# Optimization experiments

Measured on AMD Instinct MI355X. Metric: run time of the kernel, lower is better.

The kernel has to match this reference:

```python
import jax, jax.numpy as jnp
import numpy as np

HEADS = 16
DIM_HEAD = 64
MAX_REL_POS = 1024   # temporal_length
TEXT_LEN = 77
IMG_SCALE = 1.0      # image_cross_attention_scale


def setup_inputs() -> dict:
    key = jax.random.key(0)
    ks = jax.random.split(key, 12)
    B, N, D = 32, 1024, 1024
    CTX = TEXT_LEN + 256
    s = 0.02
    return {
        "x": jax.random.normal(ks[0], (B, N, D), jnp.float32),
        "context": jax.random.normal(ks[1], (B, CTX, D), jnp.float32),
        "W_q": jax.random.normal(ks[2], (D, D), jnp.float32) * s,
        "W_k": jax.random.normal(ks[3], (D, D), jnp.float32) * s,
        "W_v": jax.random.normal(ks[4], (D, D), jnp.float32) * s,
        "W_k_ip": jax.random.normal(ks[5], (D, D), jnp.float32) * s,
        "W_v_ip": jax.random.normal(ks[6], (D, D), jnp.float32) * s,
        "rel_k": jax.random.normal(ks[7], (2 * MAX_REL_POS + 1, DIM_HEAD), jnp.float32) * s,
        "rel_v": jax.random.normal(ks[8], (2 * MAX_REL_POS + 1, DIM_HEAD), jnp.float32) * s,
        "W_out": jax.random.normal(ks[9], (D, D), jnp.float32) * s,
        "b_out": jnp.zeros((D,), jnp.float32),
        "alpha": jnp.zeros((1,), jnp.float32),
    }


def _split_heads(t):
    # [b, n, h*d] -> [b, h, n, d]
    b, n, _ = t.shape
    return t.reshape(b, n, HEADS, DIM_HEAD).transpose(0, 2, 1, 3)


def _merge_heads(t):
    # [b, h, n, d] -> [b, n, h*d]
    b, h, n, d = t.shape
    return t.transpose(0, 2, 1, 3).reshape(b, n, h * d)


def _rel_embeddings(table, len_q, len_k):
    # gather relative-position embeddings: [len_q, len_k, d]
    dist = jnp.arange(len_k)[None, :] - jnp.arange(len_q)[:, None]
    idx = jnp.clip(dist, -MAX_REL_POS, MAX_REL_POS) + MAX_REL_POS
    return table[idx]


def reference(x, context, W_q, W_k, W_v, W_k_ip, W_v_ip, rel_k, rel_v, W_out, b_out, alpha):
    scale = DIM_HEAD ** -0.5
    ctx_text = context[:, :TEXT_LEN, :]
    ctx_img = context[:, TEXT_LEN:, :]

    q = _split_heads(x @ W_q)          # [b,h,i,d]
    k = _split_heads(ctx_text @ W_k)   # [b,h,j,d]
    v = _split_heads(ctx_text @ W_v)

    sim = jnp.einsum('bhid,bhjd->bhij', q, k) * scale
    len_q, len_k = q.shape[2], k.shape[2]
    k2 = _rel_embeddings(rel_k, len_q, len_k)            # [i,j,d]
    sim = sim + jnp.einsum('bhid,ijd->bhij', q, k2) * scale
    attn = jax.nn.softmax(sim, axis=-1)

    out = jnp.einsum('bhij,bhjd->bhid', attn, v)
    v2 = _rel_embeddings(rel_v, len_q, len_k)            # [i,j,d]
    out = out + jnp.einsum('bhij,ijd->bhid', attn, v2)
    out = _merge_heads(out)                              # [b,i,h*d]

    # second image-context KV stream
    k_ip = _split_heads(ctx_img @ W_k_ip)
    v_ip = _split_heads(ctx_img @ W_v_ip)
    sim_ip = jnp.einsum('bhid,bhjd->bhij', q, k_ip) * scale
    attn_ip = jax.nn.softmax(sim_ip, axis=-1)
    out_ip = _merge_heads(jnp.einsum('bhij,bhjd->bhid', attn_ip, v_ip))

    # learnable-scale bypass: out + scale * out_ip * (tanh(alpha)+1)
    out = out + IMG_SCALE * out_ip * (jnp.tanh(alpha[0]) + 1.0)
    return out @ W_out + b_out
```

## Files before the change

### kernel.cpp

```cpp
#include <hip/hip_runtime.h>
#include <math.h>

typedef __bf16 bf16_t;
typedef __bf16 bf16x2 __attribute__((ext_vector_type(2)));
typedef __bf16 bf16x8 __attribute__((ext_vector_type(8)));
typedef float f32x4 __attribute__((ext_vector_type(4)));

#define BATCH   32
#define SEQ     1024
#define DMODEL  1024
#define NHEADS  16
#define DIMH    64
#define TEXTLEN 77
#define IMGLEN  256
#define CTXLEN  333
#define MAXREL  1024

#define MFMA16(a,b,c) __builtin_amdgcn_mfma_f32_16x16x32_bf16(a, b, c, 0, 0, 0)
#define SCALE_LOG2E 0.1803368809f

__device__ __forceinline__ unsigned pk2(float a, float b) {
  union { bf16x2 v; unsigned u; } t;
  t.v[0] = (bf16_t)a; t.v[1] = (bf16_t)b;
  return t.u;
}

__global__ __launch_bounds__(128) void k_cvt_ctx(const float* __restrict__ ctx,
                                                 bf16_t* __restrict__ ctxT,
                                                 bf16_t* __restrict__ ctxI) {
  int row = blockIdx.x;
  int b = row / CTXLEN, t = row - b * CTXLEN;
  const float* src = ctx + (size_t)row * DMODEL + threadIdx.x * 8;
  bf16_t* dst = (t < TEXTLEN)
      ? ctxT + ((size_t)(b * 80 + t)) * DMODEL + threadIdx.x * 8
      : ctxI + ((size_t)(b * IMGLEN + (t - TEXTLEN))) * DMODEL + threadIdx.x * 8;
  float4 a = *(const float4*)(src);
  float4 c = *(const float4*)(src + 4);
  bf16x8 o;
  o[0] = (bf16_t)a.x; o[1] = (bf16_t)a.y; o[2] = (bf16_t)a.z; o[3] = (bf16_t)a.w;
  o[4] = (bf16_t)c.x; o[5] = (bf16_t)c.y; o[6] = (bf16_t)c.z; o[7] = (bf16_t)c.w;
  *(bf16x8*)dst = o;
  if (t == 0) {
    bf16x8 z = {};
    #pragma unroll
    for (int rr = 77; rr < 80; ++rr)
      *(bf16x8*)(ctxT + ((size_t)(b * 80 + rr)) * DMODEL + threadIdx.x * 8) = z;
  }
}

__global__ void k_transpose_w(const float* __restrict__ W, bf16_t* __restrict__ WT) {
  __shared__ float tile[32][33];
  int x = threadIdx.x, y = threadIdx.y;
  int n0 = blockIdx.x * 32, k0 = blockIdx.y * 32;
  #pragma unroll
  for (int r = 0; r < 32; r += 8)
    tile[y + r][x] = W[(size_t)(k0 + y + r) * DMODEL + n0 + x];
  __syncthreads();
  #pragma unroll
  for (int r = 0; r < 32; r += 8)
    WT[(size_t)(n0 + y + r) * DMODEL + k0 + x] = (bf16_t)tile[x][y + r];
}

__global__ __launch_bounds__(256) void k_cvt_relk(const float* __restrict__ relk,
                                                  bf16_t* __restrict__ Rkb) {
  int idx = blockIdx.x * 256 + threadIdx.x;
  int u = idx >> 3, d0 = (idx & 7) * 8;
  const float* s = relk + (size_t)(u + 1) * DIMH + d0;
  float4 a = *(const float4*)s;
  float4 b = *(const float4*)(s + 4);
  bf16x8 o;
  o[0] = (bf16_t)a.x; o[1] = (bf16_t)a.y; o[2] = (bf16_t)a.z; o[3] = (bf16_t)a.w;
  o[4] = (bf16_t)b.x; o[5] = (bf16_t)b.y; o[6] = (bf16_t)b.z; o[7] = (bf16_t)b.w;
  *(bf16x8*)(Rkb + (size_t)u * DIMH + d0) = o;
}

__global__ __launch_bounds__(256) void k_cvt_relvT(const float* __restrict__ relv,
                                                   bf16_t* __restrict__ RvT) {
  int idx = blockIdx.x * 256 + threadIdx.x;
  int d = idx >> 8, u0 = (idx & 255) * 8;
  bf16x8 o;
  #pragma unroll
  for (int e = 0; e < 8; ++e)
    o[e] = (bf16_t)relv[(size_t)(u0 + e + 1) * DIMH + d];
  *(bf16x8*)(RvT + (size_t)d * 2048 + u0) = o;
}

typedef __attribute__((address_space(1))) void gvoid;
typedef __attribute__((address_space(3))) void svoid;

__device__ __forceinline__ void async_ld16(const void* g, void* l) {
  __builtin_amdgcn_global_load_lds((gvoid*)g, (svoid*)l, 16, 0, 0);
}

template<int STORE, bool AF32, bool AHM>
__global__ __launch_bounds__(256) void k_gemm(
    const void* __restrict__ Ain, const bf16_t* __restrict__ BT,
    void* __restrict__ Cout, void* __restrict__ Cout2,
    const float* __restrict__ bias, int M, int N, int K)
{
  constexpr int ABYTES = AF32 ? 16384 : 8192;
  __shared__ __align__(16) char lds_a[ABYTES];
  __shared__ __align__(16) bf16_t lds_b[128 * 32];
  const int tid = threadIdx.x;
  const int wid = tid >> 6, lane = tid & 63;
  const int nx = gridDim.x, ny = gridDim.y;
  const int lin = blockIdx.y * nx + blockIdx.x;
  const int nwg = nx * ny;
  const int swz = (lin & 7) * (nwg >> 3) + (lin >> 3);
  const int bcol = (swz % ny) * 128;
  const int brow = (swz / ny) * 128;
  const int wr = (wid >> 1) * 64, wc = (wid & 1) * 64;
  const int lhi = lane >> 4, llo = lane & 15;

  f32x4 acc[4][4];
  #pragma unroll
  for (int m = 0; m < 4; ++m)
    #pragma unroll
    for (int n = 0; n < 4; ++n)
      acc[m][n] = (f32x4){0.f, 0.f, 0.f, 0.f};

  for (int kk = 0; kk < K; kk += 32) {
    if constexpr (AF32) {
      const float* A32 = (const float*)Ain;
      #pragma unroll
      for (int q = 0; q < 4; ++q) {
        int base = q * 4096 + wid * 1024;
        int L = base + lane * 16;
        int row = L >> 7, col16 = (L >> 4) & 7;
        async_ld16(A32 + (size_t)(brow + row) * K + kk + ((col16 ^ (row & 7)) << 2),
                   lds_a + base);
      }
    } else if constexpr (AHM) {
      const bf16_t* A16 = (const bf16_t*)Ain;
      const int hh = kk >> 6;
      #pragma unroll
      for (int ch = 0; ch < 2; ++ch) {
        int e = wid * 512 + ch * 2048 + lane * 8;
        int row = e >> 5, col = e & 31;
        int grow = brow + row;
        const bf16_t* src = A16
            + (((size_t)((grow >> 10) * 16 + hh) * 1024 + (grow & 1023)) << 6)
            + (kk & 32) + col;
        async_ld16(src, lds_a + (size_t)(wid * 512 + ch * 2048) * 2);
      }
    } else {
      const bf16_t* A16 = (const bf16_t*)Ain;
      #pragma unroll
      for (int ch = 0; ch < 2; ++ch) {
        int e = wid * 512 + ch * 2048 + lane * 8;
        int row = e >> 5, col = e & 31;
        async_ld16(A16 + (size_t)(brow + row) * K + kk + col,
                   lds_a + (size_t)(wid * 512 + ch * 2048) * 2);
      }
    }
    #pragma unroll
    for (int ch = 0; ch < 2; ++ch) {
      int e = wid * 512 + ch * 2048 + lane * 8;
      int row = e >> 5, col = e & 31;
      async_ld16(BT + (size_t)(bcol + row) * K + kk + col, &lds_b[wid * 512 + ch * 2048]);
    }
    __syncthreads();
    bf16x8 af[4], bfv[4];
    if constexpr (AF32) {
      #pragma unroll
      for (int m = 0; m < 4; ++m) {
        int row = wr + m * 16 + llo;
        int sw = (llo & 7) << 4;
        const char* rp = lds_a + row * 128;
        f32x4 a0 = *(const f32x4*)(rp + (((lhi * 2) << 4) ^ sw));
        f32x4 a1 = *(const f32x4*)(rp + (((lhi * 2 + 1) << 4) ^ sw));
        bf16x8 v;
        v[0] = (bf16_t)a0[0]; v[1] = (bf16_t)a0[1]; v[2] = (bf16_t)a0[2]; v[3] = (bf16_t)a0[3];
        v[4] = (bf16_t)a1[0]; v[5] = (bf16_t)a1[1]; v[6] = (bf16_t)a1[2]; v[7] = (bf16_t)a1[3];
        af[m] = v;
      }
    } else {
      #pragma unroll
      for (int m = 0; m < 4; ++m)
        af[m] = *(const bf16x8*)(lds_a + (size_t)((wr + m * 16 + llo) * 32 + lhi * 8) * 2);
    }
    #pragma unroll
    for (int n = 0; n < 4; ++n)
      bfv[n] = *(const bf16x8*)&lds_b[(wc + n * 16 + llo) * 32 + lhi * 8];
    #pragma unroll
    for (int m = 0; m < 4; ++m)
      #pragma unroll
      for (int n = 0; n < 4; ++n)
        acc[m][n] = MFMA16(af[m], bfv[n], acc[m][n]);
    __syncthreads();
  }

  #pragma unroll
  for (int m = 0; m < 4; ++m)
    #pragma unroll
    for (int n = 0; n < 4; ++n) {
      const int gc = bcol + wc + n * 16 + llo;
      #pragma unroll
      for (int r = 0; r < 4; ++r) {
        const int gr = brow + wr + m * 16 + lhi * 4 + r;
        float v = acc[m][n][r];
        if constexpr (STORE == 2) {
          ((float*)Cout)[(size_t)gr * N + gc] = v + bias[gc];
        } else if constexpr (STORE == 4) {
          int hh2 = gc >> 6;
          ((bf16_t*)Cout)[((((size_t)((gr >> 10) * 16 + hh2)) << 10) + (gr & 1023)) * 64
                          + (gc & 63)] = (bf16_t)v;
        } else if constexpr (STORE == 5) {
          int bb = (gr * 6554) >> 19;
          int jj = gr - bb * 80;
          int hh2 = (gc & 1023) >> 6;
          bf16_t* dst = (gc < 1024) ? (bf16_t*)Cout : (bf16_t*)Cout2;
          dst[(((size_t)(bb * 16 + hh2) * 80 + jj) << 6) + (gc & 63)] = (bf16_t)v;
        } else {
          int bb = gr >> 8, uu = gr & 255;
          int hh2 = (gc & 1023) >> 6;
          bf16_t* dst = (gc < 1024) ? (bf16_t*)Cout : (bf16_t*)Cout2;
          dst[((((size_t)(bb * 16 + hh2)) << 8) + uu) * 64 + (gc & 63)] = (bf16_t)v;
        }
      }
    }
}

template<int RPB, int OUTC>
__global__ __launch_bounds__(256) void k_vtrans(const bf16_t* __restrict__ V,
                                                bf16_t* __restrict__ Vt) {
  __shared__ bf16_t tile[64][72];
  const int nt = (OUTC + 63) / 64;
  const int u0 = (blockIdx.x % nt) * 64;
  const int bh = blockIdx.x / nt;
  const int tid = threadIdx.x;
  const int ur = tid >> 2, cg = (tid & 3) * 16;
  {
    const bf16_t* src = V + (((size_t)bh * RPB + u0 + ur) << 6) + cg;
    *(bf16x8*)&tile[ur][cg] = *(const bf16x8*)src;
    *(bf16x8*)&tile[ur][cg + 8] = *(const bf16x8*)(src + 8);
  }
  __syncthreads();
  bf16x8 o0, o1;
  #pragma unroll
  for (int e = 0; e < 8; ++e) { o0[e] = tile[cg + e][ur]; o1[e] = tile[cg + 8 + e][ur]; }
  bf16_t* dst = Vt + (size_t)bh * 64 * OUTC + (size_t)ur * OUTC + u0 + cg;
  if (u0 + cg + 8 <= OUTC)  *(bf16x8*)dst = o0;
  if (u0 + cg + 16 <= OUTC) *(bf16x8*)(dst + 8) = o1;
}

__global__ __launch_bounds__(256, 2) void k_txt(
    const bf16_t* __restrict__ Qh,
    const bf16_t* __restrict__ Kth,
    const bf16_t* __restrict__ Vtt,
    const bf16_t* __restrict__ Rkb,
    const bf16_t* __restrict__ RvT,
    bf16_t* __restrict__ Oh)
{
  __shared__ __align__(16) bf16_t kt_l[80 * 64];
  __shared__ __align__(16) bf16_t vt_l[64 * 80];
  __shared__ __align__(16) char p_l[4][6400];
  __shared__ __align__(16) char qlds[4][2048];
  __shared__ __align__(16) char olds[4][2048];
  const int tid = threadIdx.x;
  const int w = tid >> 6, lane = tid & 63;
  const int c = lane & 15, g = lane >> 4;
  const int bh = blockIdx.x;

  #pragma unroll
  for (int q = 0; q < 3; ++q) {
    int cid0 = q * 256 + w * 64;
    if (cid0 < 640) {
      int cid = cid0 + lane;
      int row = cid >> 3, cc = cid & 7;
      const bf16_t* src = Kth + (((size_t)bh * 80 + row) << 6) + ((cc ^ (row & 7)) << 3);
      async_ld16(src, (char*)kt_l + cid0 * 16);
    }
  }
  #pragma unroll
  for (int q = 0; q < 3; ++q) {
    int cid0 = q * 256 + w * 64;
    if (cid0 < 640) {
      int cid = cid0 + lane;
      int row = cid / 10;
      int col = cid - row * 10;
      int colp = col - (row & 7); if (colp < 0) colp += 10;
      const bf16_t* src = Vtt + (size_t)bh * 5120 + row * 80 + colp * 8;
      async_ld16(src, (char*)vt_l + cid0 * 16);
    }
  }
  {
    int iq = w * 256;
    #pragma unroll
    for (int k2 = 0; k2 < 2; ++k2) {
      int k = k2 * 64 + lane, rr = k >> 3, cc = k & 7;
      async_ld16(Qh + (((size_t)bh * 1024 + iq + rr) << 6) + ((cc ^ (rr & 7)) << 3),
                 qlds[w] + k2 * 1024);
    }
  }
  __syncthreads();

  bf16_t* p = (bf16_t*)p_l[w];

  for (int st = 0; st < 16; ++st) {
    const int iq = w * 256 + st * 16;
    const int ub = 1008 - iq;
    asm volatile("s_waitcnt vmcnt(0)" ::: "memory");
    bf16x8 qa0 = *(const bf16x8*)(qlds[w] + c * 128 + ((g ^ (c & 7)) << 4));
    bf16x8 qa1 = *(const bf16x8*)(qlds[w] + c * 128 + (((g + 4) ^ (c & 7)) << 4));
    asm volatile("s_waitcnt lgkmcnt(0)" ::: "memory");
    if (st < 15) {
      int iqn = iq + 16;
      #pragma unroll
      for (int k2 = 0; k2 < 2; ++k2) {
        int k = k2 * 64 + lane, rr = k >> 3, cc = k & 7;
        async_ld16(Qh + (((size_t)bh * 1024 + iqn + rr) << 6) + ((cc ^ (rr & 7)) << 3),
                   qlds[w] + k2 * 1024);
      }
    }
    f32x4 ta[6];
    #pragma unroll
    for (int n = 0; n < 6; ++n) ta[n] = (f32x4){0.f, 0.f, 0.f, 0.f};
    {
      const bf16_t* rp = Rkb + (size_t)(ub + c) * DIMH + g * 8;
      #pragma unroll
      for (int n = 0; n < 6; ++n) {
        bf16x8 b0 = *(const bf16x8*)(rp + n * 16 * DIMH);
        bf16x8 b1 = *(const bf16x8*)(rp + n * 16 * DIMH + 32);
        ta[n] = MFMA16(qa0, b0, ta[n]);
        ta[n] = MFMA16(qa1, b1, ta[n]);
      }
    }
    f32x4 s[5];
    #pragma unroll
    for (int n = 0; n < 5; ++n) s[n] = (f32x4){0.f, 0.f, 0.f, 0.f};
    {
      const int sw = (c & 7) << 4;
      #pragma unroll
      for (int n = 0; n < 5; ++n) {
        int rb = (n * 16 + c) * 128;
        bf16x8 k0 = *(const bf16x8*)((const char*)kt_l + rb + ((g << 4) ^ sw));
        bf16x8 k1 = *(const bf16x8*)((const char*)kt_l + rb + (((4 + g) << 4) ^ sw));
        s[n] = MFMA16(qa0, k0, s[n]);
        s[n] = MFMA16(qa1, k1, s[n]);
      }
    }
    float st4[5][4];
    #pragma unroll
    for (int r = 0; r < 4; ++r) {
      int il = 4 * g + r;
      int cz = c + 15 - il;
      int srcl = (lane & 48) | (cz & 15);
      bool lo_pick = (cz >> 4) == 0;
      #pragma unroll
      for (int n = 0; n < 5; ++n) {
        float tlo = __shfl(ta[n][r], srcl);
        float thi = __shfl(ta[n + 1][r], srcl);
        float tv = lo_pick ? tlo : thi;
        int j = 16 * n + c;
        st4[n][r] = (j < TEXTLEN) ? (s[n][r] + tv) : -1e30f;
      }
    }
    float rsum[4];
    #pragma unroll
    for (int r = 0; r < 4; ++r) {
      float m = st4[0][r];
      #pragma unroll
      for (int n = 1; n < 5; ++n) m = fmaxf(m, st4[n][r]);
      m = fmaxf(m, __shfl_xor(m, 1));
      m = fmaxf(m, __shfl_xor(m, 2));
      m = fmaxf(m, __shfl_xor(m, 4));
      m = fmaxf(m, __shfl_xor(m, 8));
      float ssum = 0.f;
      #pragma unroll
      for (int n = 0; n < 5; ++n) {
        float pv = exp2f((st4[n][r] - m) * SCALE_LOG2E);
        st4[n][r] = pv;
        ssum += pv;
      }
      ssum += __shfl_xor(ssum, 1);
      ssum += __shfl_xor(ssum, 2);
      ssum += __shfl_xor(ssum, 4);
      ssum += __shfl_xor(ssum, 8);
      rsum[r] = ssum;
    }
    {
      bf16x8 z8 = {};
      #pragma unroll
      for (int z = 0; z < 7; ++z) {
        int off = z * 1024 + lane * 16;
        if (off < 6400)
          *(bf16x8*)((char*)p + off) = z8;
      }
      #pragma unroll
      for (int n = 0; n < 5; ++n)
        #pragma unroll
        for (int r = 0; r < 4; ++r) {
          int j = 16 * n + c;
          if (j < TEXTLEN) {
            int il = 4 * g + r;
            bf16_t pb = (bf16_t)st4[n][r];
            p[il * 200 + (j + 15 - il)] = pb;
            p[il * 200 + 96 + j] = pb;
          }
        }
    }
    f32x4 ot[4];
    #pragma unroll
    for (int dt = 0; dt < 4; ++dt) ot[dt] = (f32x4){0.f, 0.f, 0.f, 0.f};
    #pragma unroll
    for (int kt = 0; kt < 6; ++kt) {
      bf16x8 pf = *(const bf16x8*)(p + c * 200 + kt * 32 + g * 8);
      int klo = kt * 32 + g * 8;
      #pragma unroll
      for (int dt = 0; dt < 4; ++dt) {
        int d = dt * 16 + c;
        bf16x8 af;
        if (klo < 96) {
          af = *(const bf16x8*)(RvT + (size_t)d * 2048 + ub + klo);
        } else {
          int uv = klo - 96;
          int chunk = (uv >> 3) + (c & 7); if (chunk >= 10) chunk -= 10;
          af = *(const bf16x8*)((const char*)vt_l + d * 160 + chunk * 16);
        }
        ot[dt] = MFMA16(af, pf, ot[dt]);
      }
    }
    int srcq = ((c >> 2) << 4) | c;
    float t0 = __shfl(rsum[0], srcq);
    float t1 = __shfl(rsum[1], srcq);
    float t2 = __shfl(rsum[2], srcq);
    float t3 = __shfl(rsum[3], srcq);
    float rs = (c & 2) ? ((c & 1) ? t3 : t2) : ((c & 1) ? t1 : t0);
    float inv = 1.f / rs;
    #pragma unroll
    for (int dt = 0; dt < 4; ++dt) {
      int chunk = dt * 2 + (g >> 1);
      char* pa = olds[w] + c * 128 + ((chunk ^ (c & 7)) << 4) + (g & 1) * 8;
      uint2 nv;
      nv.x = pk2(ot[dt][0] * inv, ot[dt][1] * inv);
      nv.y = pk2(ot[dt][2] * inv, ot[dt][3] * inv);
      *(uint2*)pa = nv;
    }
    char* ob = (char*)(Oh + (((size_t)bh * 1024 + iq) << 6));
    #pragma unroll
    for (int k2 = 0; k2 < 2; ++k2) {
      int k = k2 * 64 + lane, rr = k >> 3, cc = k & 7;
      uint4 v = *(uint4*)(olds[w] + rr * 128 + ((cc ^ (rr & 7)) << 4));
      *(uint4*)(ob + rr * 128 + cc * 16) = v;
    }
  }
}

__global__ __launch_bounds__(256, 2) void k_img(
    const bf16_t* __restrict__ Qh,
    const bf16_t* __restrict__ Khi,
    const bf16_t* __restrict__ Vipt,
    const float* __restrict__ alpha,
    bf16_t* __restrict__ Oh)
{
  __shared__ __align__(16) bf16_t kst[256 * 64];
  __shared__ __align__(16) bf16_t vst[64 * 256];
  __shared__ __align__(16) char qlds[4][2048];
  __shared__ __align__(16) char olds[4][2048];
  const int tid = threadIdx.x;
  const int w = tid >> 6, lane = tid & 63;
  const int c = lane & 15, g = lane >> 4;
  const int i0 = blockIdx.x * 512;
  const int bh = blockIdx.y;

  #pragma unroll
  for (int q = 0; q < 8; ++q) {
    int cid = q * 256 + tid;
    int row = cid >> 3, cc = cid & 7;
    const bf16_t* src = Khi + (((size_t)bh * 256 + row) << 6) + ((cc ^ (row & 7)) << 3);
    async_ld16(src, (char*)kst + q * 4096 + w * 1024);
  }
  const char* vsrc0 = (const char*)(Vipt + (size_t)bh * 16384);
  #pragma unroll
  for (int q = 0; q < 8; ++q) {
    int L = (q * 256 + tid) * 16;
    int row = L >> 9;
    async_ld16(vsrc0 + (L ^ ((row & 7) << 4)), (char*)vst + q * 4096 + w * 1024);
  }
  {
    int iq = i0 + w * 128;
    #pragma unroll
    for (int k2 = 0; k2 < 2; ++k2) {
      int k = k2 * 64 + lane, rr = k >> 3, cc = k & 7;
      size_t off = (((size_t)bh * 1024 + iq + rr) << 6) + ((cc ^ (rr & 7)) << 3);
      async_ld16(Qh + off, qlds[w] + k2 * 1024);
      async_ld16(Oh + off, olds[w] + k2 * 1024);
    }
  }
  __syncthreads();

  const float coef = tanhf(alpha[0]) + 1.0f;

  for (int st = 0; st < 8; ++st) {
    const int iq = i0 + w * 128 + st * 16;
    asm volatile("s_waitcnt vmcnt(0)" ::: "memory");
    bf16x8 qa0 = *(const bf16x8*)(qlds[w] + c * 128 + ((g ^ (c & 7)) << 4));
    bf16x8 qa1 = *(const bf16x8*)(qlds[w] + c * 128 + (((g + 4) ^ (c & 7)) << 4));
    asm volatile("s_waitcnt lgkmcnt(0)" ::: "memory");
    if (st < 7) {
      int iqn = iq + 16;
      #pragma unroll
      for (int k2 = 0; k2 < 2; ++k2) {
        int k = k2 * 64 + lane, rr = k >> 3, cc = k & 7;
        async_ld16(Qh + (((size_t)bh * 1024 + iqn + rr) << 6) + ((cc ^ (rr & 7)) << 3),
                   qlds[w] + k2 * 1024);
      }
    }
    f32x4 acc[4];
    #pragma unroll
    for (int dt = 0; dt < 4; ++dt) acc[dt] = (f32x4){0.f, 0.f, 0.f, 0.f};
    float m_run = -1e30f, l_run = 0.f;

    #pragma unroll
    for (int jt = 0; jt < 2; ++jt) {
      f32x4 s2[8];
      #pragma unroll
      for (int n = 0; n < 8; ++n) s2[n] = (f32x4){0.f, 0.f, 0.f, 0.f};
      const int sw = (c & 7) << 4;
      #pragma unroll
      for (int n = 0; n < 8; ++n) {
        int rb = (jt * 128 + n * 16 + c) * 128;
        bf16x8 k0 = *(const bf16x8*)((const char*)kst + rb + ((g << 4) ^ sw));
        bf16x8 k1 = *(const bf16x8*)((const char*)kst + rb + (((4 + g) << 4) ^ sw));
        s2[n] = MFMA16(k0, qa0, s2[n]);
        s2[n] = MFMA16(k1, qa1, s2[n]);
      }
      float mx = -1e30f;
      #pragma unroll
      for (int n = 0; n < 8; ++n)
        #pragma unroll
        for (int r = 0; r < 4; ++r) mx = fmaxf(mx, s2[n][r]);
      mx = fmaxf(mx, __shfl_xor(mx, 16));
      mx = fmaxf(mx, __shfl_xor(mx, 32));
      float m_new = fmaxf(m_run, mx);
      float fscale = exp2f((m_run - m_new) * SCALE_LOG2E);
      float tsum = 0.f;
      #pragma unroll
      for (int n = 0; n < 8; ++n)
        #pragma unroll
        for (int r = 0; r < 4; ++r) {
          float pv = exp2f((s2[n][r] - m_new) * SCALE_LOG2E);
          s2[n][r] = pv; tsum += pv;
        }
      tsum += __shfl_xor(tsum, 16);
      tsum += __shfl_xor(tsum, 32);
      l_run = l_run * fscale + tsum;
      m_run = m_new;
      #pragma unroll
      for (int dt = 0; dt < 4; ++dt) acc[dt] *= fscale;
      const int srcA = c | ((g & 1) << 5);
      const int srcB = srcA + 16;
      const bool hi_n = ((g >> 1) & 1) != 0;
      #pragma unroll
      for (int kt = 0; kt < 4; ++kt) {
        unsigned lo0 = pk2(s2[2 * kt][0], s2[2 * kt][1]);
        unsigned hi0 = pk2(s2[2 * kt][2], s2[2 * kt][3]);
        unsigned lo1 = pk2(s2[2 * kt + 1][0], s2[2 * kt + 1][1]);
        unsigned hi1 = pk2(s2[2 * kt + 1][2], s2[2 * kt + 1][3]);
        unsigned a0 = __shfl(lo0, srcA), a1 = __shfl(lo1, srcA);
        unsigned b0 = __shfl(hi0, srcA), b1 = __shfl(hi1, srcA);
        unsigned c0 = __shfl(lo0, srcB), c1 = __shfl(lo1, srcB);
        unsigned d0 = __shfl(hi0, srcB), d1 = __shfl(hi1, srcB);
        union { unsigned u[4]; bf16x8 v; } pf;
        pf.u[0] = hi_n ? a1 : a0;
        pf.u[1] = hi_n ? b1 : b0;
        pf.u[2] = hi_n ? c1 : c0;
        pf.u[3] = hi_n ? d1 : d0;
        #pragma unroll
        for (int dt = 0; dt < 4; ++dt) {
          int d = dt * 16 + c;
          int a = (d * 512 + jt * 256 + kt * 64 + g * 16) ^ ((c & 7) << 4);
          bf16x8 vf = *(const bf16x8*)((const char*)vst + a);
          acc[dt] = MFMA16(vf, pf.v, acc[dt]);
        }
      }
    }
    float inv = coef / l_run;
    asm volatile("s_waitcnt vmcnt(0)" ::: "memory");
    #pragma unroll
    for (int dt = 0; dt < 4; ++dt) {
      int chunk = dt * 2 + (g >> 1);
      char* pa = olds[w] + c * 128 + ((chunk ^ (c & 7)) << 4) + (g & 1) * 8;
      union { uint2 u2; bf16_t e[4]; } ov; ov.u2 = *(uint2*)pa;
      uint2 nv;
      nv.x = pk2((float)ov.e[0] + acc[dt][0] * inv, (float)ov.e[1] + acc[dt][1] * inv);
      nv.y = pk2((float)ov.e[2] + acc[dt][2] * inv, (float)ov.e[3] + acc[dt][3] * inv);
      *(uint2*)pa = nv;
    }
    char* ob = (char*)(Oh + (((size_t)bh * 1024 + iq) << 6));
    #pragma unroll
    for (int k2 = 0; k2 < 2; ++k2) {
      int k = k2 * 64 + lane, rr = k >> 3, cc = k & 7;
      uint4 v = *(uint4*)(olds[w] + rr * 128 + ((cc ^ (rr & 7)) << 4));
      *(uint4*)(ob + rr * 128 + cc * 16) = v;
    }
    asm volatile("s_waitcnt lgkmcnt(0)" ::: "memory");
    if (st < 7) {
      int iqn = iq + 16;
      #pragma unroll
      for (int k2 = 0; k2 < 2; ++k2) {
        int k = k2 * 64 + lane, rr = k >> 3, cc = k & 7;
        async_ld16(Oh + (((size_t)bh * 1024 + iqn + rr) << 6) + ((cc ^ (rr & 7)) << 3),
                   olds[w] + k2 * 1024);
      }
    }
  }
}

extern "C" void kernel_launch(void* const* d_in, const int* in_sizes, int n_in,
                              void* d_out, int out_size, void* d_ws, size_t ws_size,
                              hipStream_t stream)
{
  const float* x     = (const float*)d_in[0];
  const float* ctx   = (const float*)d_in[1];
  const float* W_q   = (const float*)d_in[2];
  const float* W_k   = (const float*)d_in[3];
  const float* W_v   = (const float*)d_in[4];
  const float* W_kip = (const float*)d_in[5];
  const float* W_vip = (const float*)d_in[6];
  const float* rel_k = (const float*)d_in[7];
  const float* rel_v = (const float*)d_in[8];
  const float* W_out = (const float*)d_in[9];
  const float* b_out = (const float*)d_in[10];
  const float* alpha = (const float*)d_in[11];

  char* ws = (char*)d_ws;
  bf16_t* Oh   = (bf16_t*)(ws + 0);
  bf16_t* Qh   = (bf16_t*)(ws + 67108864);
  bf16_t* CtxT = (bf16_t*)(ws + 134217728);
  bf16_t* CtxI = (bf16_t*)(ws + 139460608);
  bf16_t* WTs  = (bf16_t*)(ws + 156237824);
  bf16_t* WqT   = WTs + 0 * 1048576;
  bf16_t* WkT   = WTs + 1 * 1048576;
  bf16_t* WvT   = WTs + 2 * 1048576;
  bf16_t* WkipT = WTs + 3 * 1048576;
  bf16_t* WvipT = WTs + 4 * 1048576;
  bf16_t* WoutT = WTs + 5 * 1048576;

  char* dob = (char*)d_out;
  bf16_t* Khi   = (bf16_t*)(dob + 0);
  bf16_t* Vhi   = (bf16_t*)(dob + 16777216);
  bf16_t* Vipt  = (bf16_t*)(dob + 33554432);
  bf16_t* Kth   = (bf16_t*)(dob + 50331648);
  bf16_t* Vth   = (bf16_t*)(dob + 55574528);
  bf16_t* Vtt   = (bf16_t*)(dob + 60817408);
  bf16_t* Rkb   = (bf16_t*)(dob + 66060288);
  bf16_t* RvT   = (bf16_t*)(dob + 66322432);

  k_cvt_ctx<<<BATCH * CTXLEN, 128, 0, stream>>>(ctx, CtxT, CtxI);
  dim3 tb(32, 8), tg(32, 32);
  k_transpose_w<<<tg, tb, 0, stream>>>(W_q,   WqT);
  k_transpose_w<<<tg, tb, 0, stream>>>(W_k,   WkT);
  k_transpose_w<<<tg, tb, 0, stream>>>(W_v,   WvT);
  k_transpose_w<<<tg, tb, 0, stream>>>(W_kip, WkipT);
  k_transpose_w<<<tg, tb, 0, stream>>>(W_vip, WvipT);
  k_transpose_w<<<tg, tb, 0, stream>>>(W_out, WoutT);
  k_cvt_relk<<<64, 256, 0, stream>>>(rel_k, Rkb);
  k_cvt_relvT<<<64, 256, 0, stream>>>(rel_v, RvT);

  k_gemm<4, true,  false><<<dim3(256, 8), 256, 0, stream>>>(x, WqT, (void*)Qh, nullptr, nullptr, 32768, 1024, 1024);
  k_gemm<5, false, false><<<dim3(20, 16), 256, 0, stream>>>(CtxT, WkT,   (void*)Kth, (void*)Vth, nullptr, 2560, 2048, 1024);
  k_gemm<6, false, false><<<dim3(64, 16), 256, 0, stream>>>(CtxI, WkipT, (void*)Khi, (void*)Vhi, nullptr, 8192, 2048, 1024);

  k_vtrans<80,  80 ><<<2 * 512, 256, 0, stream>>>(Vth, Vtt);
  k_vtrans<256, 256><<<4 * 512, 256, 0, stream>>>(Vhi, Vipt);

  k_txt<<<512, 256, 0, stream>>>(Qh, Kth, Vtt, Rkb, RvT, Oh);
  k_img<<<dim3(2, 512), 256, 0, stream>>>(Qh, Khi, Vipt, alpha, Oh);

  k_gemm<2, false, true><<<dim3(256, 8), 256, 0, stream>>>(Oh, WoutT, d_out, nullptr, b_out, 32768, 1024, 1024);
}
```

Measured before the change: 583.1 us.

## Double-buffer LDS tiles in GEMM to overlap global loads with MFMA

The GEMM kernel now keeps two LDS buffers for the A and B tiles and issues the async global-to-LDS loads for the next K step before computing on the current one. Explicit vmcnt waits, matched to the number of outstanding loads per stage, replace the full syncthreads, so memory latency can overlap MFMA work. This doubles LDS use per block, which may lower occupancy, and it relies on hand-counted waitcnt values being correct.

```diff
diff --git a/kernel.cpp b/kernel.cpp
--- a/kernel.cpp
+++ b/kernel.cpp
@@ -99,8 +99,8 @@
     const float* __restrict__ bias, int M, int N, int K)
 {
   constexpr int ABYTES = AF32 ? 16384 : 8192;
-  __shared__ __align__(16) char lds_a[ABYTES];
-  __shared__ __align__(16) bf16_t lds_b[128 * 32];
+  __shared__ __align__(16) char lds_a[2][ABYTES];
+  __shared__ __align__(16) bf16_t lds_b[2][128 * 32];
   const int tid = threadIdx.x;
   const int wid = tid >> 6, lane = tid & 63;
   const int nx = gridDim.x, ny = gridDim.y;
@@ -112,14 +112,8 @@
   const int wr = (wid >> 1) * 64, wc = (wid & 1) * 64;
   const int lhi = lane >> 4, llo = lane & 15;
 
-  f32x4 acc[4][4];
-  #pragma unroll
-  for (int m = 0; m < 4; ++m)
-    #pragma unroll
-    for (int n = 0; n < 4; ++n)
-      acc[m][n] = (f32x4){0.f, 0.f, 0.f, 0.f};
-
-  for (int kk = 0; kk < K; kk += 32) {
+  auto stage = [&](int kk, int buf) __attribute__((always_inline)) {
+    char* la = lds_a[buf];
     if constexpr (AF32) {
       const float* A32 = (const float*)Ain;
       #pragma unroll
@@ -128,7 +122,7 @@
         int L = base + lane * 16;
         int row = L >> 7, col16 = (L >> 4) & 7;
         async_ld16(A32 + (size_t)(brow + row) * K + kk + ((col16 ^ (row & 7)) << 2),
-                   lds_a + base);
+                   la + base);
       }
     } else if constexpr (AHM) {
       const bf16_t* A16 = (const bf16_t*)Ain;
@@ -141,7 +135,7 @@
         const bf16_t* src = A16
             + (((size_t)((grow >> 10) * 16 + hh) * 1024 + (grow & 1023)) << 6)
             + (kk & 32) + col;
-        async_ld16(src, lds_a + (size_t)(wid * 512 + ch * 2048) * 2);
+        async_ld16(src, la + (size_t)(wid * 512 + ch * 2048) * 2);
       }
     } else {
       const bf16_t* A16 = (const bf16_t*)Ain;
@@ -150,23 +144,48 @@
         int e = wid * 512 + ch * 2048 + lane * 8;
         int row = e >> 5, col = e & 31;
         async_ld16(A16 + (size_t)(brow + row) * K + kk + col,
-                   lds_a + (size_t)(wid * 512 + ch * 2048) * 2);
-      }
-    }
+                   la + (size_t)(wid * 512 + ch * 2048) * 2);
+      }
+    }
+    bf16_t* lb = lds_b[buf];
     #pragma unroll
     for (int ch = 0; ch < 2; ++ch) {
       int e = wid * 512 + ch * 2048 + lane * 8;
       int row = e >> 5, col = e & 31;
-      async_ld16(BT + (size_t)(bcol + row) * K + kk + col, &lds_b[wid * 512 + ch * 2048]);
-    }
-    __syncthreads();
+      async_ld16(BT + (size_t)(bcol + row) * K + kk + col, &lb[wid * 512 + ch * 2048]);
+    }
+  };
+
+  f32x4 acc[4][4];
+  #pragma unroll
+  for (int m = 0; m < 4; ++m)
+    #pragma unroll
+    for (int n = 0; n < 4; ++n)
+      acc[m][n] = (f32x4){0.f, 0.f, 0.f, 0.f};
+
+  stage(0, 0);
+  int cur = 0;
+  for (int kk = 0; kk < K; kk += 32) {
+    if (kk + 32 < K) {
+      stage(kk + 32, cur ^ 1);
+      __builtin_amdgcn_sched_barrier(0);
+      if constexpr (AF32)
+        asm volatile("s_waitcnt vmcnt(6)" ::: "memory");
+      else
+        asm volatile("s_waitcnt vmcnt(4)" ::: "memory");
+      __builtin_amdgcn_sched_barrier(0);
+    } else {
+      asm volatile("s_waitcnt vmcnt(0)" ::: "memory");
+    }
+    __builtin_amdgcn_s_barrier();
+
     bf16x8 af[4], bfv[4];
     if constexpr (AF32) {
       #pragma unroll
       for (int m = 0; m < 4; ++m) {
         int row = wr + m * 16 + llo;
         int sw = (llo & 7) << 4;
-        const char* rp = lds_a + row * 128;
+        const char* rp = lds_a[cur] + row * 128;
         f32x4 a0 = *(const f32x4*)(rp + (((lhi * 2) << 4) ^ sw));
         f32x4 a1 = *(const f32x4*)(rp + (((lhi * 2 + 1) << 4) ^ sw));
         bf16x8 v;
@@ -177,17 +196,21 @@
     } else {
       #pragma unroll
       for (int m = 0; m < 4; ++m)
-        af[m] = *(const bf16x8*)(lds_a + (size_t)((wr + m * 16 + llo) * 32 + lhi * 8) * 2);
+        af[m] = *(const bf16x8*)(lds_a[cur] + (size_t)((wr + m * 16 + llo) * 32 + lhi * 8) * 2);
     }
     #pragma unroll
     for (int n = 0; n < 4; ++n)
-      bfv[n] = *(const bf16x8*)&lds_b[(wc + n * 16 + llo) * 32 + lhi * 8];
+      bfv[n] = *(const bf16x8*)&lds_b[cur][(wc + n * 16 + llo) * 32 + lhi * 8];
     #pragma unroll
     for (int m = 0; m < 4; ++m)
       #pragma unroll
       for (int n = 0; n < 4; ++n)
         acc[m][n] = MFMA16(af[m], bfv[n], acc[m][n]);
-    __syncthreads();
+
+    asm volatile("s_waitcnt lgkmcnt(0)" ::: "memory");
+    __builtin_amdgcn_sched_barrier(0);
+    __builtin_amdgcn_s_barrier();
+    cur ^= 1;
   }
 
   #pragma unroll
```

Measured after the change: 569.5 us. 2.3% less time.
